# Kernel optimization log

Hardware: AMD Instinct MI355X
Metric: run time of the kernel (lower is better)

Reference implementation:

```python
import jax, jax.numpy as jnp
import numpy as np

D_CONV = 4
D_STATE = 32
DT_RANK = 16


def setup_inputs() -> dict:
    key = jax.random.key(0)
    ks = jax.random.split(key, 12)
    B, D, L, DI = 4, 256, 1024, 256
    s = 0.02
    return {
        "x": jax.random.normal(ks[0], (B, D, L), jnp.float32),
        "Win": jax.random.normal(ks[1], (4, D, 2 * DI), jnp.float32) * s,
        "Wconv": jax.random.normal(ks[2], (4, DI, D_CONV), jnp.float32) * 0.2,
        "bconv": jnp.zeros((4, DI), jnp.float32),
        "Wxp": jax.random.normal(ks[3], (4, DI, DT_RANK + 2 * D_STATE), jnp.float32) * s,
        "Wdt": jax.random.normal(ks[4], (4, DT_RANK, DI), jnp.float32) * s,
        "bdt": jnp.full((4, DI), -2.0, jnp.float32),
        "Alog": jnp.tile(jnp.log(jnp.arange(1, D_STATE + 1, dtype=jnp.float32))[None, None, :], (4, DI, 1)),
        "Dskip": jnp.ones((4, DI), jnp.float32),
        "Wout": jax.random.normal(ks[5], (4, DI, D), jnp.float32) * s,
        "Wg": jax.random.normal(ks[6], (2, L, L), jnp.float32) * 0.01,
        "bg": jnp.zeros((2, L), jnp.float32),
        "alpha": jnp.ones((2,), jnp.float32),
        "gamma": jnp.ones((2, L), jnp.float32),
        "beta": jnp.zeros((2, L), jnp.float32),
    }


def _selective_scan(u, dt, Bm, Cm, A):
    # u, dt: [B,L,di]; Bm, Cm: [B,L,N]; A: [di,N]
    dBu = dt * u
    def step(h, inp):
        dt_t, dbu_t, B_t, C_t = inp  # [B,di],[B,di],[B,N],[B,N]
        h = jnp.exp(dt_t[:, :, None] * A) * h + dbu_t[:, :, None] * B_t[:, None, :]
        y = jnp.einsum('bdn,bn->bd', h, C_t)
        return h, y
    xs = (jnp.moveaxis(dt, 1, 0), jnp.moveaxis(dBu, 1, 0),
          jnp.moveaxis(Bm, 1, 0), jnp.moveaxis(Cm, 1, 0))
    h0 = jnp.zeros((u.shape[0], A.shape[0], A.shape[1]), u.dtype)
    _, ys = jax.lax.scan(step, h0, xs)  # ys: [L,B,di]
    return jnp.moveaxis(ys, 0, 1)


def _mamba_layer(x_bdl, Win, Wconv, bconv, Wxp, Wdt, bdt, Alog, Dskip, Wout):
    x = jnp.swapaxes(x_bdl, 1, 2)  # [B,L,D]
    L = x.shape[1]
    u, z = jnp.split(x @ Win, 2, axis=-1)  # each [B,L,di]
    up = jnp.pad(u, ((0, 0), (D_CONV - 1, 0), (0, 0)))
    u = sum(up[:, k:k + L, :] * Wconv[:, k] for k in range(D_CONV)) + bconv
    u = jax.nn.silu(u)
    proj = u @ Wxp
    dtp = proj[..., :DT_RANK]
    Bm = proj[..., DT_RANK:DT_RANK + D_STATE]
    Cm = proj[..., DT_RANK + D_STATE:]
    dt = jax.nn.softplus(dtp @ Wdt + bdt)
    y = _selective_scan(u, dt, Bm, Cm, -jnp.exp(Alog)) + u * Dskip
    y = y * jax.nn.silu(z)
    return jnp.swapaxes(y @ Wout, 1, 2)  # [B,d_out,L]


def _forward(x, Win, Wconv, bconv, Wxp, Wdt, bdt, Alog, Dskip, Wout, Wg, bg, alpha, gamma, beta):
    def branch(inp, i0, i1, j):
        h = _mamba_layer(inp, Win[i0], Wconv[i0], bconv[i0], Wxp[i0], Wdt[i0], bdt[i0], Alog[i0], Dskip[i0], Wout[i0])
        h = _mamba_layer(h, Win[i1], Wconv[i1], bconv[i1], Wxp[i1], Wdt[i1], bdt[i1], Alog[i1], Dskip[i1], Wout[i1])
        return gamma[j] * jnp.tanh(alpha[j] * h) + beta[j]  # DyTanh over last dim
    def gate(j):
        return jax.nn.sigmoid(jnp.einsum('bdl,ml->bdm', x, Wg[j]) + bg[j])
    m = branch(x, 0, 1, 0) * gate(0)
    rx = jnp.flip(x, axis=-1)
    rm = branch(rx, 2, 3, 1) * gate(1)
    return m + jnp.flip(rm, axis=-1)


def reference(x, Win, Wconv, bconv, Wxp, Wdt, bdt, Alog, Dskip, Wout, Wg, bg, alpha, gamma, beta):
    return _forward(x, Win, Wconv, bconv, Wxp, Wdt, bdt, Alog, Dskip, Wout, Wg, bg, alpha, gamma, beta)
```

## Files before the change

kernel.cpp:

```cpp
#include <hip/hip_runtime.h>


#define LSEQ 1024
#define SCAN_CL 16
#define SCAN_NC 64
#define G1PLANE 2097152L

#if __has_builtin(__builtin_amdgcn_exp2f)
#define EXP2(x) __builtin_amdgcn_exp2f(x)
#else
#define EXP2(x) exp2f(x)
#endif

typedef short bf16x8 __attribute__((ext_vector_type(8)));
typedef float f32x4 __attribute__((ext_vector_type(4)));

__device__ __forceinline__ float sigmoidf_(float x) { return 1.f / (1.f + __expf(-x)); }
__device__ __forceinline__ float siluf_(float x)    { return x / (1.f + __expf(-x)); }
__device__ __forceinline__ float softplusf_(float x){ return x > 20.f ? x : log1pf(__expf(x)); }

__device__ __forceinline__ unsigned short bf16rne_(float v) {
  unsigned u = __float_as_uint(v);
  return (unsigned short)((u + 0x7FFFu + ((u >> 16) & 1u)) >> 16);
}
__device__ __forceinline__ float bfto_(unsigned short h) {
  return __uint_as_float(((unsigned)h) << 16);
}
__device__ __forceinline__ void split3_(float v, unsigned short& h,
                                        unsigned short& m, unsigned short& l) {
  h = bf16rne_(v); float r = v - bfto_(h);
  m = bf16rne_(r); float r2 = r - bfto_(m);
  l = bf16rne_(r2);
}

__device__ __forceinline__ long swzi(long idx, long row) {
  return idx ^ (((row >> 1) & 3) << 3);
}

__device__ void tconv3_body(const float* __restrict__ in,
                            unsigned short* __restrict__ oh,
                            unsigned short* __restrict__ om,
                            unsigned short* __restrict__ ol,
                            int K, int N, int bx, int by, int z) {
  __shared__ float T[32][33];
  int n0 = bx * 32, k0 = by * 32;
  int tx = threadIdx.x & 31, ty = threadIdx.x >> 5;
  const float* src = in + (long)z * K * N;
#pragma unroll
  for (int m = 0; m < 4; ++m)
    T[ty + 8 * m][tx] = src[(long)(k0 + ty + 8 * m) * N + n0 + tx];
  __syncthreads();
  long obase = (long)z * N * K;
#pragma unroll
  for (int m = 0; m < 4; ++m) {
    float v = T[tx][ty + 8 * m];
    int n = n0 + ty + 8 * m;
    long o = swzi(obase + (long)n * K + k0 + tx, n);
    split3_(v, oh[o], om[o], ol[o]);
  }
}

__device__ void split3v_body(const float4* __restrict__ in,
                             unsigned short* __restrict__ oh,
                             unsigned short* __restrict__ om,
                             unsigned short* __restrict__ ol, int i) {
  float4 v = in[i];
  long b = 4L * i;
  long sb = swzi(b, b >> 10);
  ushort4 H, M, L;
  split3_(v.x, H.x, M.x, L.x); split3_(v.y, H.y, M.y, L.y);
  split3_(v.z, H.z, M.z, L.z); split3_(v.w, H.w, M.w, L.w);
  *(ushort4*)(oh + sb) = H; *(ushort4*)(om + sb) = M; *(ushort4*)(ol + sb) = L;
}

__global__ __launch_bounds__(256)
void preprocess_kernel(const float* __restrict__ x, const float* __restrict__ Wg,
                       const float* __restrict__ Win, const float* __restrict__ Wout,
                       const float* __restrict__ Alog,
                       unsigned short* __restrict__ Xh, unsigned short* __restrict__ Xm,
                       unsigned short* __restrict__ Xl,
                       unsigned short* __restrict__ XGh, unsigned short* __restrict__ XGm,
                       unsigned short* __restrict__ XGl,
                       unsigned short* __restrict__ Wgh, unsigned short* __restrict__ Wgm,
                       unsigned short* __restrict__ Wgl,
                       unsigned short* __restrict__ WinTh, unsigned short* __restrict__ WinTm,
                       unsigned short* __restrict__ WinTl,
                       unsigned short* __restrict__ WoutTh, unsigned short* __restrict__ WoutTm,
                       unsigned short* __restrict__ WoutTl,
                       float* __restrict__ Aneg) {
  const int bid = blockIdx.x;
  if (bid < 8192) {
    long idx = (long)bid * 256 + threadIdx.x;
    int d = (int)(idx & 255);
    long t = idx >> 8;
    int l = (int)(t & 1023);
    int t2 = (int)(t >> 10);
    int b = t2 & 3;
    int j = t2 >> 2;
    int lsrc = j ? (1023 - l) : l;
    float v = x[((long)(b * 256 + d)) * LSEQ + lsrc];
    long o = swzi(idx, t);
    split3_(v, Xh[o], Xm[o], Xl[o]);
  } else if (bid < 9216) {
    int i = (bid - 8192) * 256 + threadIdx.x;
    split3v_body((const float4*)x, XGh, XGm, XGl, i);
  } else if (bid < 11264) {
    int i = (bid - 9216) * 256 + threadIdx.x;
    split3v_body((const float4*)Wg, Wgh, Wgm, Wgl, i);
  } else if (bid < 11776) {
    int t = bid - 11264;
    tconv3_body(Win, WinTh, WinTm, WinTl, 256, 512, t & 15, (t >> 4) & 7, t >> 7);
  } else if (bid < 12032) {
    int t = bid - 11776;
    tconv3_body(Wout, WoutTh, WoutTm, WoutTl, 256, 256, t & 7, (t >> 3) & 7, t >> 6);
  } else {
    int idx = (bid - 12032) * 256 + threadIdx.x;
    Aneg[idx] = -__expf(Alog[idx]) * 1.4426950408889634f;
  }
}

__device__ __forceinline__ void gload16(const unsigned short* g, unsigned short* l) {
  __builtin_amdgcn_global_load_lds(
      (const __attribute__((address_space(1))) unsigned int*)g,
      (__attribute__((address_space(3))) unsigned int*)l, 16, 0, 0);
}

template <int KSPLIT>
__global__ __launch_bounds__(256)
void gemm_mfma(const unsigned short* __restrict__ Ah_g,
               const unsigned short* __restrict__ Am_g,
               const unsigned short* __restrict__ Al_g, long aZ, int lda,
               const unsigned short* __restrict__ Bh_g,
               const unsigned short* __restrict__ Bm_g,
               const unsigned short* __restrict__ Bl_g, long bZ, int ldb,
               float* __restrict__ C, long cZ, int N, int KH) {
  __shared__ unsigned short S[6][128 * 32];
  const int bz = blockIdx.z;
  const int z  = bz / KSPLIT;
  const int kh = bz % KSPLIT;
  const int m0 = blockIdx.y * 128, n0 = blockIdx.x * 128;
  const int tid = threadIdx.x;

  const long khoff = (long)kh * KH;
  const long a0 = (long)z * aZ + (long)(m0 + (tid >> 2)) * lda + khoff + (tid & 3) * 8;
  const long a1 = a0 + 64L * lda;
  const long b0 = (long)z * bZ + (long)(n0 + (tid >> 2)) * ldb + khoff + (tid & 3) * 8;
  const long b1 = b0 + 64L * ldb;
  const int l0 = tid * 8, l1 = tid * 8 + 2048;

  const int lane = tid & 63, w = tid >> 6;
  const int wr = w >> 1, wc = w & 1;
  const int fr = lane & 15, g = lane >> 4;

  f32x4 acc[4][4];
#pragma unroll
  for (int i = 0; i < 4; ++i)
#pragma unroll
    for (int j = 0; j < 4; ++j)
#pragma unroll
      for (int q = 0; q < 4; ++q) acc[i][j][q] = 0.f;

  for (int k0 = 0; k0 < KH; k0 += 32) {
    __syncthreads();
    gload16(Ah_g + a0 + k0, &S[0][l0]); gload16(Ah_g + a1 + k0, &S[0][l1]);
    gload16(Am_g + a0 + k0, &S[1][l0]); gload16(Am_g + a1 + k0, &S[1][l1]);
    gload16(Al_g + a0 + k0, &S[2][l0]); gload16(Al_g + a1 + k0, &S[2][l1]);
    gload16(Bh_g + b0 + k0, &S[3][l0]); gload16(Bh_g + b1 + k0, &S[3][l1]);
    gload16(Bm_g + b0 + k0, &S[4][l0]); gload16(Bm_g + b1 + k0, &S[4][l1]);
    gload16(Bl_g + b0 + k0, &S[5][l0]); gload16(Bl_g + b1 + k0, &S[5][l1]);
    __syncthreads();

    bf16x8 fb[3][4];
#pragma unroll
    for (int nf = 0; nf < 4; ++nf) {
      int rb = wc * 64 + nf * 16 + fr;
      int ob = rb * 32 + ((g ^ ((rb >> 1) & 3)) << 3);
      fb[0][nf] = *(const bf16x8*)&S[3][ob];
      fb[1][nf] = *(const bf16x8*)&S[4][ob];
      fb[2][nf] = *(const bf16x8*)&S[5][ob];
    }
#pragma unroll
    for (int mf = 0; mf < 4; ++mf) {
      int ra = wr * 64 + mf * 16 + fr;
      int oa = ra * 32 + ((g ^ ((ra >> 1) & 3)) << 3);
      bf16x8 fah = *(const bf16x8*)&S[0][oa];
      bf16x8 fam = *(const bf16x8*)&S[1][oa];
      bf16x8 fal = *(const bf16x8*)&S[2][oa];
#pragma unroll
      for (int nf = 0; nf < 4; ++nf) {
        acc[mf][nf] = __builtin_amdgcn_mfma_f32_16x16x32_bf16(fah, fb[0][nf], acc[mf][nf], 0, 0, 0);
        acc[mf][nf] = __builtin_amdgcn_mfma_f32_16x16x32_bf16(fah, fb[1][nf], acc[mf][nf], 0, 0, 0);
        acc[mf][nf] = __builtin_amdgcn_mfma_f32_16x16x32_bf16(fam, fb[0][nf], acc[mf][nf], 0, 0, 0);
        acc[mf][nf] = __builtin_amdgcn_mfma_f32_16x16x32_bf16(fam, fb[1][nf], acc[mf][nf], 0, 0, 0);
        acc[mf][nf] = __builtin_amdgcn_mfma_f32_16x16x32_bf16(fah, fb[2][nf], acc[mf][nf], 0, 0, 0);
        acc[mf][nf] = __builtin_amdgcn_mfma_f32_16x16x32_bf16(fal, fb[0][nf], acc[mf][nf], 0, 0, 0);
      }
    }
  }

  float* Cz = C + (long)bz * cZ;
#pragma unroll
  for (int mf = 0; mf < 4; ++mf)
#pragma unroll
    for (int nf = 0; nf < 4; ++nf) {
      int col = n0 + wc * 64 + nf * 16 + fr;
      int row0 = m0 + wr * 64 + mf * 16 + g * 4;
#pragma unroll
      for (int q = 0; q < 4; ++q)
        Cz[(long)(row0 + q) * N + col] = acc[mf][nf][q];
    }
}

template <int OP, int NP>
__global__ __launch_bounds__(256)
void combineN_kernel(const float* __restrict__ P, long pz,
                     const float* __restrict__ bias, int nmask,
                     float* __restrict__ outF,
                     unsigned short* __restrict__ oh,
                     unsigned short* __restrict__ om,
                     unsigned short* __restrict__ ol, long oz) {
  int z = blockIdx.y;
  long i = (long)blockIdx.x * 256 + threadIdx.x;
  float v = 0.f;
#pragma unroll
  for (int p = 0; p < NP; ++p) v += P[(long)(z * NP + p) * pz + i];
  if (OP == 1) {
    outF[(long)z * oz + i] = sigmoidf_(v + bias[z * (nmask + 1) + (int)(i & nmask)]);
  } else if (OP == 0) {
    outF[(long)z * oz + i] = v;
  } else {
    long o = (long)z * oz + swzi(i, i >> 8);
    split3_(v, oh[o], om[o], ol[o]);
  }
}

__global__ __launch_bounds__(256)
void gemm23_kernel(const float* __restrict__ UC, const float* __restrict__ Wxp,
                   const float* __restrict__ Wdt, const float* __restrict__ bdt,
                   float* __restrict__ PROJ, float* __restrict__ DTo, int stage) {
  __shared__ float As[16][17];
  __shared__ float Ws[16][80];
  __shared__ float PR[16][17];
  __shared__ float WD[16][256];
  const int z = blockIdx.y;
  const int lidx = stage + 2 * z;
  const int m0 = blockIdx.x * 16;
  const long abase = (long)z * 4096 * 256 + (long)m0 * 256;
  const float* W = Wxp + (long)lidx * 256 * 80;
  const int tid = threadIdx.x;
  const int tx = tid & 15, ty = tid >> 4;

#pragma unroll
  for (int t = 0; t < 16; ++t) {
    int e = t * 256 + tid;
    WD[e >> 8][e & 255] = Wdt[(long)lidx * 4096 + e];
  }

  float acc[5];
#pragma unroll
  for (int j = 0; j < 5; ++j) acc[j] = 0.f;

  for (int k0 = 0; k0 < 256; k0 += 16) {
    As[tx][ty] = UC[abase + (long)ty * 256 + k0 + tx];
    {
      int k = tid >> 4, cg2 = (tid & 15) * 5;
#pragma unroll
      for (int i2 = 0; i2 < 5; ++i2)
        Ws[k][cg2 + i2] = W[(long)(k0 + k) * 80 + cg2 + i2];
    }
    __syncthreads();
#pragma unroll
    for (int kk = 0; kk < 16; ++kk) {
      float a = As[kk][ty];
#pragma unroll
      for (int j = 0; j < 5; ++j)
        acc[j] = fmaf(a, Ws[kk][tx * 5 + j], acc[j]);
    }
    __syncthreads();
  }

#pragma unroll
  for (int j = 0; j < 5; ++j) {
    int c = tx * 5 + j;
    float v = acc[j];
    PROJ[((long)z * 4096 + m0 + ty) * 80 + c] = v;
    if (c < 16) PR[ty][c] = v;
  }
  __syncthreads();

  for (int it = 0; it < 16; ++it) {
    float ssum = 0.f;
#pragma unroll
    for (int k = 0; k < 16; ++k) ssum = fmaf(PR[it][k], WD[k][tid], ssum);
    DTo[((long)z * 4096 + m0 + it) * 256 + tid] =
        softplusf_(ssum + bdt[lidx * 256 + tid]);
  }
}

__global__ __launch_bounds__(256) void conv_kernel(const float* __restrict__ PG1,
                                                   const float* __restrict__ Wconv,
                                                   const float* __restrict__ bconv,
                                                   float* __restrict__ uc, int stage) {
  long idx = (long)blockIdx.x * 256 + threadIdx.x;
  int di = (int)(idx & 255);
  long r = idx >> 8;
  int l = (int)(r & 1023);
  int j = (int)(r >> 12);
  int lidx = stage + 2 * j;
  const float* wc = Wconv + (long)(lidx * 256 + di) * 4;
  float acc = bconv[lidx * 256 + di];
  long rr = r & 4095;
  const float* u0 = PG1 + (long)(j * 2) * G1PLANE + (rr - 3) * 512 + di;
  const float* u1 = u0 + G1PLANE;
  if (l >= 3) {
    acc = fmaf(u0[0]    + u1[0],    wc[0], acc);
    acc = fmaf(u0[512]  + u1[512],  wc[1], acc);
    acc = fmaf(u0[1024] + u1[1024], wc[2], acc);
    acc = fmaf(u0[1536] + u1[1536], wc[3], acc);
  } else {
    for (int k = 3 - l; k < 4; ++k)
      acc = fmaf(u0[(long)k * 512] + u1[(long)k * 512], wc[k], acc);
  }
  uc[idx] = acc * sigmoidf_(acc);
}

template <int PASS>
__global__ __launch_bounds__(256)
void scan_chunk_kernel(const float* __restrict__ dt,
                       const float* __restrict__ uc,
                       const float* __restrict__ PG1,
                       const float* __restrict__ proj,
                       const float* __restrict__ Aneg,
                       const float* __restrict__ Dskip,
                       float* __restrict__ HST,
                       float* __restrict__ DTS,
                       unsigned short* __restrict__ YGh,
                       unsigned short* __restrict__ YGm,
                       unsigned short* __restrict__ YGl, int stage) {
  __shared__ __align__(16) float BC[SCAN_CL][64];
  const int blk = blockIdx.x;
  const int chunk = blk & (SCAN_NC - 1);
  const int jb = blk >> 6;
  const int di = threadIdx.x;
  const int j = jb >> 2;
  const int lidx = stage + 2 * j;
  const long r0 = (long)jb * 1024 + (long)chunk * SCAN_CL;

  for (int e = threadIdx.x; e < SCAN_CL * 64; e += 256) {
    int l = e >> 6, col = e & 63;
    BC[l][col] = proj[(r0 + l) * 80 + 16 + col];
  }

  float A[32];
  {
    const float4* ap = (const float4*)(Aneg + ((long)(lidx * 256 + di)) * 32);
#pragma unroll
    for (int q = 0; q < 8; ++q) {
      float4 v = ap[q];
      A[4 * q] = v.x; A[4 * q + 1] = v.y; A[4 * q + 2] = v.z; A[4 * q + 3] = v.w;
    }
  }

  const long sbase = (((long)jb * SCAN_NC + chunk) * 256 + di) * 32;
  float h[32];
  if (PASS == 0) {
#pragma unroll
    for (int n = 0; n < 32; ++n) h[n] = 0.f;
  } else {
    const float4* hp = (const float4*)(HST + sbase);
#pragma unroll
    for (int q = 0; q < 8; ++q) {
      float4 v = hp[q];
      h[4 * q] = v.x; h[4 * q + 1] = v.y; h[4 * q + 2] = v.z; h[4 * q + 3] = v.w;
    }
  }

  float Dsk = 0.f, dtsum = 0.f;
  if (PASS == 1) Dsk = Dskip[lidx * 256 + di];

  const float* dtp = dt + r0 * 256 + di;
  const float* up  = uc + r0 * 256 + di;
  const float* zp0 = PG1 + (long)(j * 2) * G1PLANE + (r0 & 4095) * 512 + 256 + di;
  const float* zp1 = zp0 + G1PLANE;

  __syncthreads();

  float Db[2][8], Ub[2][8], Zb[2][8];
#pragma unroll
  for (int i = 0; i < 8; ++i) {
    Db[0][i] = dtp[(long)i * 256];
    Ub[0][i] = up[(long)i * 256];
    if (PASS == 1) Zb[0][i] = zp0[(long)i * 512] + zp1[(long)i * 512];
  }

#pragma unroll
  for (int bt = 0; bt < SCAN_CL / 8; ++bt) {
    const int cur = bt & 1, nxt = cur ^ 1;
    if (bt < SCAN_CL / 8 - 1) {
#pragma unroll
      for (int i = 0; i < 8; ++i) {
        long l = (long)(bt + 1) * 8 + i;
        Db[nxt][i] = dtp[l * 256];
        Ub[nxt][i] = up[l * 256];
        if (PASS == 1) Zb[nxt][i] = zp0[l * 512] + zp1[l * 512];
      }
    }
#pragma unroll
    for (int i = 0; i < 8; ++i) {
      const int l = bt * 8 + i;
      float dtv = Db[cur][i];
      float uv  = Ub[cur][i];
      float du  = dtv * uv;
      if (PASS == 0) dtsum += dtv;
      float yacc[4] = {0.f, 0.f, 0.f, 0.f};
      const float4* bc4 = (const float4*)&BC[l][0];
#pragma unroll
      for (int q = 0; q < 8; ++q) {
        float4 bv = bc4[q];
        float4 cv = bc4[8 + q];
        const float* bp = &bv.x;
        const float* cp = &cv.x;
#pragma unroll
        for (int k = 0; k < 4; ++k) {
          int n = 4 * q + k;
          float a = EXP2(dtv * A[n]);
          h[n] = fmaf(a, h[n], du * bp[k]);
          yacc[n & 3] = fmaf(h[n], cp[k], yacc[n & 3]);
        }
      }
      if (PASS == 1) {
        float y = (yacc[0] + yacc[1]) + (yacc[2] + yacc[3]);
        float zv = Zb[cur][i];
        float val = (y + uv * Dsk) * siluf_(zv);
        long o = swzi((r0 + l) * 256 + di, r0 + l);
        split3_(val, YGh[o], YGm[o], YGl[o]);
      }
    }
  }

  if (PASS == 0) {
    float4* hp = (float4*)(HST + sbase);
#pragma unroll
    for (int q = 0; q < 8; ++q)
      hp[q] = make_float4(h[4 * q], h[4 * q + 1], h[4 * q + 2], h[4 * q + 3]);
    DTS[((long)jb * SCAN_NC + chunk) * 256 + di] = dtsum;
  }
}

__global__ __launch_bounds__(256)
void scan_combine_kernel(float* __restrict__ HST, const float* __restrict__ DTS,
                         const float* __restrict__ Aneg, int stage) {
  int t = blockIdx.x * 256 + threadIdx.x;
  int n = t & 31;
  int di = (t >> 5) & 255;
  int jb = t >> 13;
  int lidx = stage + 2 * (jb >> 2);
  float A = Aneg[((long)(lidx * 256 + di)) * 32 + n];
  float hs = 0.f;
  for (int cb = 0; cb < SCAN_NC; cb += 8) {
    float s[8], P[8], hv[8];
#pragma unroll
    for (int i = 0; i < 8; ++i) {
      long base = ((long)jb * SCAN_NC + cb + i) * 256 + di;
      s[i] = HST[base * 32 + n];
      P[i] = DTS[base];
    }
#pragma unroll
    for (int i = 0; i < 8; ++i) P[i] = EXP2(A * P[i]);
#pragma unroll
    for (int i = 0; i < 8; ++i) {
      hv[i] = hs;
      hs = fmaf(P[i], hs, s[i]);
    }
#pragma unroll
    for (int i = 0; i < 8; ++i) {
      long base = ((long)jb * SCAN_NC + cb + i) * 256 + di;
      HST[base * 32 + n] = hv[i];
    }
  }
}

__global__ __launch_bounds__(256) void combine_kernel(const float* __restrict__ H,
                                                      const float* __restrict__ gate,
                                                      const float* __restrict__ alpha,
                                                      const float* __restrict__ gamma,
                                                      const float* __restrict__ beta,
                                                      float* __restrict__ out) {
  long idx = (long)blockIdx.x * 256 + threadIdx.x;
  int l = (int)(idx & 1023);
  long t = idx >> 10;
  int d = (int)(t & 255);
  int b = (int)(t >> 8);
  int lr = 1023 - l;
  float h0 = H[(((long)b * 1024 + l) * 256) + d];
  float h1 = H[(((long)(4 + b) * 1024 + lr) * 256) + d];
  float g0 = gate[((long)(b * 256 + d)) * 1024 + l];
  float g1 = gate[(long)1024 * 1024 + ((long)(b * 256 + d)) * 1024 + lr];
  float m0 = (gamma[l] * tanhf(alpha[0] * h0) + beta[l]) * g0;
  float m1 = (gamma[1024 + lr] * tanhf(alpha[1] * h1) + beta[1024 + lr]) * g1;
  out[idx] = m0 + m1;
}

extern "C" void kernel_launch(void* const* d_in, const int* in_sizes, int n_in,
                              void* d_out, int out_size, void* d_ws, size_t ws_size,
                              hipStream_t stream) {
  const float* x     = (const float*)d_in[0];
  const float* Win   = (const float*)d_in[1];
  const float* Wconv = (const float*)d_in[2];
  const float* bconv = (const float*)d_in[3];
  const float* Wxp   = (const float*)d_in[4];
  const float* Wdt   = (const float*)d_in[5];
  const float* bdt   = (const float*)d_in[6];
  const float* Alog  = (const float*)d_in[7];
  const float* Dskip = (const float*)d_in[8];
  const float* Wout  = (const float*)d_in[9];
  const float* Wg    = (const float*)d_in[10];
  const float* bg    = (const float*)d_in[11];
  const float* alpha = (const float*)d_in[12];
  const float* gamma = (const float*)d_in[13];
  const float* beta  = (const float*)d_in[14];
  float* out = (float*)d_out;

  float* ws   = (float*)d_ws;
  float* UC   = ws;
  float* PROJ = UC + 2097152;
  float* DT   = PROJ + 655360;
  float* GATE = DT + 2097152;
  float* ANEG = GATE + 2097152;
  float* HST  = ANEG + 32768;
  float* DTS  = HST + 4194304;
  float* XF   = DTS + 131072;
  float* PG   = XF + 2097152;
  unsigned short* Xpl  = (unsigned short*)(PG + 8388608);
  unsigned short* YGpl = Xpl + 3 * 2097152;
  unsigned short* XGpl = YGpl + 3 * 2097152;
  unsigned short* Wgpl = XGpl + 3 * 1048576;
  unsigned short* WinT = Wgpl + 3 * 2097152;
  unsigned short* WoutT = WinT + 3 * 524288;
  unsigned short* Xh = Xpl, *Xm = Xpl + 2097152, *Xl = Xpl + 2 * 2097152;
  unsigned short* YGh = YGpl, *YGm = YGpl + 2097152, *YGl = YGpl + 2 * 2097152;
  unsigned short* XGh = XGpl, *XGm = XGpl + 1048576, *XGl = XGpl + 2 * 1048576;
  unsigned short* Wgh = Wgpl, *Wgm = Wgpl + 2097152, *Wgl = Wgpl + 2 * 2097152;
  unsigned short* WinTh = WinT, *WinTm = WinT + 524288, *WinTl = WinT + 2 * 524288;
  unsigned short* WoutTh = WoutT, *WoutTm = WoutT + 262144, *WoutTl = WoutT + 2 * 262144;

  preprocess_kernel<<<dim3(12160), dim3(256), 0, stream>>>(
      x, Wg, Win, Wout, Alog, Xh, Xm, Xl, XGh, XGm, XGl,
      Wgh, Wgm, Wgl, WinTh, WinTm, WinTl, WoutTh, WoutTm, WoutTl, ANEG);

  gemm_mfma<4><<<dim3(8, 8, 8), dim3(256), 0, stream>>>(
      XGh, XGm, XGl, 0L, 1024,
      Wgh, Wgm, Wgl, (long)1024 * 1024, 1024,
      PG, (long)1024 * 1024, 1024, 256);
  combineN_kernel<1, 4><<<dim3(4096, 2), dim3(256), 0, stream>>>(
      PG, (long)1024 * 1024, bg, 1023, GATE, nullptr, nullptr, nullptr,
      (long)1024 * 1024);

  for (int s = 0; s < 2; ++s) {
    gemm_mfma<2><<<dim3(4, 32, 4), dim3(256), 0, stream>>>(
        Xh, Xm, Xl, (long)4096 * 256, 256,
        WinTh + (long)s * 131072, WinTm + (long)s * 131072, WinTl + (long)s * 131072,
        (long)262144, 256,
        PG, G1PLANE, 512, 128);

    conv_kernel<<<dim3(8192), dim3(256), 0, stream>>>(PG, Wconv, bconv, UC, s);

    gemm23_kernel<<<dim3(256, 2), dim3(256), 0, stream>>>(
        UC, Wxp, Wdt, bdt, PROJ, DT, s);

    scan_chunk_kernel<0><<<dim3(8 * SCAN_NC), dim3(256), 0, stream>>>(
        DT, UC, PG, PROJ, ANEG, Dskip, HST, DTS, YGh, YGm, YGl, s);
    scan_combine_kernel<<<dim3(256), dim3(256), 0, stream>>>(HST, DTS, ANEG, s);
    scan_chunk_kernel<1><<<dim3(8 * SCAN_NC), dim3(256), 0, stream>>>(
        DT, UC, PG, PROJ, ANEG, Dskip, HST, DTS, YGh, YGm, YGl, s);

    gemm_mfma<2><<<dim3(2, 32, 4), dim3(256), 0, stream>>>(
        YGh, YGm, YGl, (long)4096 * 256, 256,
        WoutTh + (long)s * 65536, WoutTm + (long)s * 65536, WoutTl + (long)s * 65536,
        (long)131072, 256,
        PG, (long)4096 * 256, 256, 128);
    if (s == 0) {
      combineN_kernel<2, 2><<<dim3(4096, 2), dim3(256), 0, stream>>>(
          PG, (long)4096 * 256, nullptr, 0, nullptr, Xh, Xm, Xl, (long)4096 * 256);
    } else {
      combineN_kernel<0, 2><<<dim3(4096, 2), dim3(256), 0, stream>>>(
          PG, (long)4096 * 256, nullptr, 0, XF, nullptr, nullptr, nullptr,
          (long)4096 * 256);
    }
  }

  combine_kernel<<<dim3(4096), dim3(256), 0, stream>>>(XF, GATE, alpha, gamma, beta, out);
}
```

Baseline: 337.0 us.

## Remap GEMM grid for XCD-aware tile placement and fuse final split-K reduction

```diff
diff --git a/kernel.cpp b/kernel.cpp
--- a/kernel.cpp
+++ b/kernel.cpp
@@ -133,12 +133,18 @@
                const unsigned short* __restrict__ Bh_g,
                const unsigned short* __restrict__ Bm_g,
                const unsigned short* __restrict__ Bl_g, long bZ, int ldb,
-               float* __restrict__ C, long cZ, int N, int KH) {
+               float* __restrict__ C, long cZ, int N, int KH,
+               int NT, int MT) {
   __shared__ unsigned short S[6][128 * 32];
-  const int bz = blockIdx.z;
+  const int wgid = blockIdx.x;
+  const int r8 = wgid & 7, q8 = wgid >> 3;
+  const int mti = q8 % MT, gHi = q8 / MT;
+  const int grp = gHi * 8 + r8;
+  const int nti = grp % NT;
+  const int bz  = grp / NT;
   const int z  = bz / KSPLIT;
   const int kh = bz % KSPLIT;
-  const int m0 = blockIdx.y * 128, n0 = blockIdx.x * 128;
+  const int m0 = mti * 128, n0 = nti * 128;
   const int tid = threadIdx.x;
 
   const long khoff = (long)kh * KH;
@@ -226,8 +232,6 @@
   for (int p = 0; p < NP; ++p) v += P[(long)(z * NP + p) * pz + i];
   if (OP == 1) {
     outF[(long)z * oz + i] = sigmoidf_(v + bias[z * (nmask + 1) + (int)(i & nmask)]);
-  } else if (OP == 0) {
-    outF[(long)z * oz + i] = v;
   } else {
     long o = (long)z * oz + swzi(i, i >> 8);
     split3_(v, oh[o], om[o], ol[o]);
@@ -480,7 +484,8 @@
   }
 }
 
-__global__ __launch_bounds__(256) void combine_kernel(const float* __restrict__ H,
+__global__ __launch_bounds__(256) void combine_kernel(const float* __restrict__ PG,
+                                                      long pz,
                                                       const float* __restrict__ gate,
                                                       const float* __restrict__ alpha,
                                                       const float* __restrict__ gamma,
@@ -492,8 +497,10 @@
   int d = (int)(t & 255);
   int b = (int)(t >> 8);
   int lr = 1023 - l;
-  float h0 = H[(((long)b * 1024 + l) * 256) + d];
-  float h1 = H[(((long)(4 + b) * 1024 + lr) * 256) + d];
+  long b0 = ((long)(b * 1024 + l)) * 256 + d;
+  long b1 = ((long)(b * 1024 + lr)) * 256 + d;
+  float h0 = PG[b0] + PG[pz + b0];
+  float h1 = PG[2 * pz + b1] + PG[3 * pz + b1];
   float g0 = gate[((long)(b * 256 + d)) * 1024 + l];
   float g1 = gate[(long)1024 * 1024 + ((long)(b * 256 + d)) * 1024 + lr];
   float m0 = (gamma[l] * tanhf(alpha[0] * h0) + beta[l]) * g0;
@@ -529,8 +536,7 @@
   float* ANEG = GATE + 2097152;
   float* HST  = ANEG + 32768;
   float* DTS  = HST + 4194304;
-  float* XF   = DTS + 131072;
-  float* PG   = XF + 2097152;
+  float* PG   = DTS + 131072;
   unsigned short* Xpl  = (unsigned short*)(PG + 8388608);
   unsigned short* YGpl = Xpl + 3 * 2097152;
   unsigned short* XGpl = YGpl + 3 * 2097152;
@@ -548,20 +554,20 @@
       x, Wg, Win, Wout, Alog, Xh, Xm, Xl, XGh, XGm, XGl,
       Wgh, Wgm, Wgl, WinTh, WinTm, WinTl, WoutTh, WoutTm, WoutTl, ANEG);
 
-  gemm_mfma<4><<<dim3(8, 8, 8), dim3(256), 0, stream>>>(
+  gemm_mfma<4><<<dim3(512), dim3(256), 0, stream>>>(
       XGh, XGm, XGl, 0L, 1024,
       Wgh, Wgm, Wgl, (long)1024 * 1024, 1024,
-      PG, (long)1024 * 1024, 1024, 256);
+      PG, (long)1024 * 1024, 1024, 256, 8, 8);
   combineN_kernel<1, 4><<<dim3(4096, 2), dim3(256), 0, stream>>>(
       PG, (long)1024 * 1024, bg, 1023, GATE, nullptr, nullptr, nullptr,
       (long)1024 * 1024);
 
   for (int s = 0; s < 2; ++s) {
-    gemm_mfma<2><<<dim3(4, 32, 4), dim3(256), 0, stream>>>(
+    gemm_mfma<2><<<dim3(512), dim3(256), 0, stream>>>(
         Xh, Xm, Xl, (long)4096 * 256, 256,
         WinTh + (long)s * 131072, WinTm + (long)s * 131072, WinTl + (long)s * 131072,
         (long)262144, 256,
-        PG, G1PLANE, 512, 128);
+        PG, G1PLANE, 512, 128, 4, 32);
 
     conv_kernel<<<dim3(8192), dim3(256), 0, stream>>>(PG, Wconv, bconv, UC, s);
 
@@ -574,20 +580,17 @@
     scan_chunk_kernel<1><<<dim3(8 * SCAN_NC), dim3(256), 0, stream>>>(
         DT, UC, PG, PROJ, ANEG, Dskip, HST, DTS, YGh, YGm, YGl, s);
 
-    gemm_mfma<2><<<dim3(2, 32, 4), dim3(256), 0, stream>>>(
+    gemm_mfma<2><<<dim3(256), dim3(256), 0, stream>>>(
         YGh, YGm, YGl, (long)4096 * 256, 256,
         WoutTh + (long)s * 65536, WoutTm + (long)s * 65536, WoutTl + (long)s * 65536,
         (long)131072, 256,
-        PG, (long)4096 * 256, 256, 128);
+        PG, (long)4096 * 256, 256, 128, 2, 32);
     if (s == 0) {
       combineN_kernel<2, 2><<<dim3(4096, 2), dim3(256), 0, stream>>>(
           PG, (long)4096 * 256, nullptr, 0, nullptr, Xh, Xm, Xl, (long)4096 * 256);
-    } else {
-      combineN_kernel<0, 2><<<dim3(4096, 2), dim3(256), 0, stream>>>(
-          PG, (long)4096 * 256, nullptr, 0, XF, nullptr, nullptr, nullptr,
-          (long)4096 * 256);
-    }
-  }
-
-  combine_kernel<<<dim3(4096), dim3(256), 0, stream>>>(XF, GATE, alpha, gamma, beta, out);
-}
+    }
+  }
+
+  combine_kernel<<<dim3(4096), dim3(256), 0, stream>>>(
+      PG, (long)4096 * 256, GATE, alpha, gamma, beta, out);
+}
```

Result: no change. 341.2 us (+1.2%).
